# Optimization experiments

Hardware: AMD Instinct MI355X
Metric: run time of the kernel (lower is better)

## Reference

```python
import jax, jax.numpy as jnp
import numpy as np

R = 32
BN_EPS = 1e-5


def _bn(x, g, b):
    # eval-mode BatchNorm with running_mean=0, running_var=1
    shp = (1, -1) + (1,) * (x.ndim - 2)
    scale = g / np.float32(np.sqrt(1.0 + BN_EPS))
    return x * scale.reshape(shp) + b.reshape(shp)


def _conv3d(x, w, b):
    y = jax.lax.conv_general_dilated(x, w, (1, 1, 1), [(1, 1)] * 3,
                                     dimension_numbers=('NCDHW', 'OIDHW', 'NCDHW'))
    return y + b[None, :, None, None, None]


def _conv1d(x, w, b):  # kernel_size=1 conv -> matmul; w [O,I], x [B,I,N]
    return jnp.einsum('oi,bin->bon', w, x) + b[None, :, None]


def _voxelize(features, coords, r):
    # PVCNN Voxelization: detach coords, center, normalize, scatter-average
    coords = jax.lax.stop_gradient(coords)
    c = coords - coords.mean(axis=2, keepdims=True)            # [B,3,N]
    nrm = jnp.linalg.norm(c, axis=1, keepdims=True)            # [B,1,N]
    c = c / (nrm.max(axis=2, keepdims=True) * 2.0) + 0.5
    c = jnp.clip(c * r, 0.0, r - 1.0)                          # float voxel coords
    vox = jnp.round(c).astype(jnp.int32)
    B, C, N = features.shape
    idx = vox[:, 0] * r * r + vox[:, 1] * r + vox[:, 2]        # [B,N]
    flat = (idx + (jnp.arange(B, dtype=jnp.int32) * (r ** 3))[:, None]).reshape(-1)
    feats = features.transpose(0, 2, 1).reshape(B * N, C)
    sums = jax.ops.segment_sum(feats, flat, num_segments=B * r ** 3)
    cnt = jax.ops.segment_sum(jnp.ones((B * N,), features.dtype), flat, num_segments=B * r ** 3)
    grid = sums / jnp.maximum(cnt, 1.0)[:, None]
    grid = grid.reshape(B, r, r, r, C).transpose(0, 4, 1, 2, 3)  # [B,C,r,r,r]
    return grid, c


def _devoxelize(grid, c, r):
    # trilinear interpolation gather at float coords c in [0, r-1]
    B, C = grid.shape[:2]
    lo = jnp.clip(jnp.floor(c).astype(jnp.int32), 0, r - 1)
    hi = jnp.minimum(lo + 1, r - 1)
    f = c - lo.astype(c.dtype)
    gridf = grid.reshape(B, C, r * r * r)
    gather = jax.vmap(lambda g, i: g[:, i])  # per-batch [C,R3],[N] -> [C,N]
    out = jnp.zeros((B, C, c.shape[2]), grid.dtype)
    for ix, wx in ((lo[:, 0], 1.0 - f[:, 0]), (hi[:, 0], f[:, 0])):
        for iy, wy in ((lo[:, 1], 1.0 - f[:, 1]), (hi[:, 1], f[:, 1])):
            for iz, wz in ((lo[:, 2], 1.0 - f[:, 2]), (hi[:, 2], f[:, 2])):
                idx = ix * r * r + iy * r + iz
                out = out + gather(gridf, idx) * (wx * wy * wz)[:, None, :]
    return out


def setup_inputs() -> dict:
    key = jax.random.key(0)
    ks = jax.random.split(key, 24)
    n = lambda k, s, sc=0.05: (jax.random.normal(k, s, dtype=jnp.float32) * sc)
    inp = {
        'features': jax.random.normal(ks[0], (4, 64, 65536), dtype=jnp.float32),
        'coords': jax.random.normal(ks[1], (4, 3, 65536), dtype=jnp.float32),
        'vconv_w': n(ks[2], (64, 64, 3, 3, 3)),
        'vconv_b': n(ks[3], (64,)),
        'vbn_g': 1.0 + n(ks[4], (64,)),
        'vbn_b': n(ks[5], (64,)),
        'res_w': n(ks[6], (2, 2, 64, 64, 3, 3, 3)),
        'res_b': n(ks[7], (2, 2, 64)),
        'res_bn_g': 1.0 + n(ks[8], (2, 2, 64)),
        'res_bn_b': n(ks[9], (2, 2, 64)),
        'pf_w': n(ks[10], (64, 64)),
        'pf_b': n(ks[11], (64,)),
        'pf_bn_g': 1.0 + n(ks[12], (64,)),
        'pf_bn_b': n(ks[13], (64,)),
        'attn_wa': n(ks[14], (16, 64)),
        'attn_ba': n(ks[15], (16,)),
        'attn_wb': n(ks[16], (16, 64)),
        'attn_bb': n(ks[17], (16,)),
        'attn_wc': n(ks[18], (1, 32)),
        'attn_bc': n(ks[19], (1,)),
    }
    return inp


def reference(features, coords, vconv_w, vconv_b, vbn_g, vbn_b,
              res_w, res_b, res_bn_g, res_bn_b,
              pf_w, pf_b, pf_bn_g, pf_bn_b,
              attn_wa, attn_ba, attn_wb, attn_bb, attn_wc, attn_bc):
    grid, nc = _voxelize(features, coords, R)
    # BasicConvolutionBlock
    x = jax.nn.relu(_bn(_conv3d(grid, vconv_w, vconv_b), vbn_g, vbn_b))
    # two ResidualBlocks (inc==outc, stride 1 -> identity downsample)
    for i in range(2):
        y = jax.nn.relu(_bn(_conv3d(x, res_w[i, 0], res_b[i, 0]), res_bn_g[i, 0], res_bn_b[i, 0]))
        y = _bn(_conv3d(y, res_w[i, 1], res_b[i, 1]), res_bn_g[i, 1], res_bn_b[i, 1])
        x = jax.nn.relu(y + x)
    vfeat = _devoxelize(x, nc, R)                               # [B,64,N]
    # SharedMLP: Conv1d(k=1) + BN1d + ReLU
    pfeat = jax.nn.relu(_bn(_conv1d(features, pf_w, pf_b), pf_bn_g, pf_bn_b))
    # Attn fusion (channel dim 64 -> atten_64 branch)
    xa = _conv1d(vfeat, attn_wa, attn_ba)
    xb = _conv1d(pfeat, attn_wb, attn_bb)
    q = _conv1d(jnp.concatenate([xa, xb], axis=1), attn_wc, attn_bc)
    attention = 1.0 + jax.nn.sigmoid(q)
    fused = vfeat * attention + pfeat
    return fused
```

## Files before the change

kernel.cpp:

```cpp
#include <hip/hip_runtime.h>
#include <math.h>

#define NPT 65536
#define NB 4
#define R3 32768

typedef __attribute__((ext_vector_type(8))) short short8;
typedef __attribute__((ext_vector_type(16))) float f32x16;

#define OFF_WB16 0
#define OFF_BEFF 276480
#define OFF_PWB  276800
#define OFF_PB   280896
#define OFF_WAE  280960
#define OFF_WBE  281024
#define OFF_Q0   281088
#define OFF_MEAN 281104
#define OFF_MAXN 281116
#define OFF_PART 281120
#define OFF_AUX  281248
#define OFF_CB3  281504
#define OFF_CUR  1067936
#define OFF_ORD  1199008
#define OFF_GA   1330080
#define OFF_G0   9718688
#define OFF_G1   13912992

__device__ __forceinline__ unsigned short f2b(float f) {
    union { float f; unsigned int u; } v; v.f = f;
    unsigned int r = v.u + 0x7fffu + ((v.u >> 16) & 1u);
    return (unsigned short)(r >> 16);
}
__device__ __forceinline__ float b2f(unsigned short u) {
    union { unsigned int u; float f; } v; v.u = ((unsigned int)u) << 16; return v.f;
}

__global__ void k_setup(const float* __restrict__ vconv_w, const float* __restrict__ vconv_b,
                        const float* __restrict__ vbn_g, const float* __restrict__ vbn_b,
                        const float* __restrict__ res_w, const float* __restrict__ res_b,
                        const float* __restrict__ res_bn_g, const float* __restrict__ res_bn_b,
                        const float* __restrict__ pf_w, const float* __restrict__ pf_b,
                        const float* __restrict__ pf_bn_g, const float* __restrict__ pf_bn_b,
                        const float* __restrict__ wa, const float* __restrict__ ba,
                        const float* __restrict__ wb, const float* __restrict__ bb,
                        const float* __restrict__ wc, const float* __restrict__ bc,
                        float* __restrict__ ws) {
    int idx = blockIdx.x * 256 + threadIdx.x;
    const float invs = rsqrtf(1.00001f);
    if (idx < 552960) {
        unsigned short* wb16 = (unsigned short*)(ws + OFF_WB16);
        int j = idx & 7;
        int l = (idx >> 3) & 63;
        int nh = (idx >> 9) & 1;
        int ks = (idx >> 10) & 3;
        int rest = idx >> 12;
        int t = rest % 27;
        int layer = rest / 27;
        int i = ks * 16 + ((l >> 5) << 3) + j;
        int o = nh * 32 + (l & 31);
        float scale, wsrc;
        if (layer == 0) {
            scale = vbn_g[o] * invs;
            wsrc = vconv_w[(o * 64 + i) * 27 + t];
        } else {
            scale = res_bn_g[(layer - 1) * 64 + o] * invs;
            wsrc = res_w[(size_t)(layer - 1) * 110592 + (o * 64 + i) * 27 + t];
        }
        wb16[idx] = f2b(wsrc * scale);
        return;
    }
    idx -= 552960;
    if (idx < 320) {
        int l = idx >> 6, o = idx & 63;
        float b_, g_, s_;
        if (l == 0) { b_ = vconv_b[o]; g_ = vbn_g[o]; s_ = vbn_b[o]; }
        else {
            b_ = res_b[(l - 1) * 64 + o];
            g_ = res_bn_g[(l - 1) * 64 + o];
            s_ = res_bn_b[(l - 1) * 64 + o];
        }
        ws[OFF_BEFF + idx] = b_ * g_ * invs + s_;
    } else if (idx < 4416) {
        int e = idx - 320;
        int j = e & 7;
        int lane = (e >> 3) & 63;
        int ks = (e >> 9) & 3;
        int half = e >> 11;
        int i = ks * 16 + ((lane >> 5) << 3) + j;
        int o = half * 32 + (lane & 31);
        ((unsigned short*)(ws + OFF_PWB))[e] = f2b(pf_w[o * 64 + i] * pf_bn_g[o] * invs);
    } else if (idx < 4480) {
        int o = idx - 4416;
        ws[OFF_PB + o] = pf_b[o] * pf_bn_g[o] * invs + pf_bn_b[o];
    } else if (idx < 4544) {
        int o = idx - 4480;
        float s = 0.f;
        for (int j = 0; j < 16; j++) s += wc[j] * wa[j * 64 + o];
        ws[OFF_WAE + o] = s;
    } else if (idx < 4608) {
        int o = idx - 4544;
        float s = 0.f;
        for (int j = 0; j < 16; j++) s += wc[16 + j] * wb[j * 64 + o];
        ws[OFF_WBE + o] = s;
    } else if (idx == 4608) {
        float s = bc[0];
        for (int j = 0; j < 16; j++) s += wc[j] * ba[j] + wc[16 + j] * bb[j];
        ws[OFF_Q0] = s;
    }
}

__global__ __launch_bounds__(256) void k_mean1(const float* __restrict__ coords,
                                               float* __restrict__ part,
                                               float4* __restrict__ curz) {
    for (int i = blockIdx.x * 256 + threadIdx.x; i < 32768; i += 96 * 256)
        curz[i] = make_float4(0.f, 0.f, 0.f, 0.f);
    __shared__ float sm[256];
    int bd = blockIdx.x >> 3, chunk = blockIdx.x & 7;
    int tid = threadIdx.x;
    const float* p = coords + (size_t)bd * NPT + chunk * 8192;
    float s = 0.f;
    for (int n = tid; n < 8192; n += 256) s += p[n];
    sm[tid] = s; __syncthreads();
    for (int st = 128; st > 0; st >>= 1) {
        if (tid < st) sm[tid] += sm[tid + st];
        __syncthreads();
    }
    if (tid == 0) part[blockIdx.x] = sm[0];
}

__global__ __launch_bounds__(256) void k_maxn1(const float* __restrict__ coords,
                                               float* __restrict__ part,
                                               float* __restrict__ mean) {
    __shared__ float sm[256];
    int b = blockIdx.x >> 3, chunk = blockIdx.x & 7;
    int tid = threadIdx.x;
    float m0 = 0.f, m1 = 0.f, m2 = 0.f;
    #pragma unroll
    for (int c = 0; c < 8; c++) {
        m0 += part[(b * 3 + 0) * 8 + c];
        m1 += part[(b * 3 + 1) * 8 + c];
        m2 += part[(b * 3 + 2) * 8 + c];
    }
    m0 *= (1.0f / NPT); m1 *= (1.0f / NPT); m2 *= (1.0f / NPT);
    if (chunk == 0 && tid == 0) {
        mean[b * 3] = m0; mean[b * 3 + 1] = m1; mean[b * 3 + 2] = m2;
    }
    const float* p0 = coords + (size_t)(b * 3) * NPT + chunk * 8192;
    float mx = 0.f;
    for (int n = tid; n < 8192; n += 256) {
        float dx = p0[n] - m0, dy = p0[NPT + n] - m1, dz = p0[2 * NPT + n] - m2;
        mx = fmaxf(mx, dx * dx + dy * dy + dz * dz);
    }
    sm[tid] = mx; __syncthreads();
    for (int st = 128; st > 0; st >>= 1) {
        if (tid < st) sm[tid] = fmaxf(sm[tid], sm[tid + st]);
        __syncthreads();
    }
    if (tid == 0) part[96 + blockIdx.x] = sm[0];
}

__global__ void k_prep(const float* __restrict__ coords, const float* __restrict__ mean,
                       const float* __restrict__ part, float* __restrict__ cb3,
                       int* __restrict__ cursor) {
    int gid = blockIdx.x * 256 + threadIdx.x;
    int b = gid >> 16, n = gid & 65535;
    float mx = 0.f;
    #pragma unroll
    for (int c = 0; c < 8; c++) mx = fmaxf(mx, part[96 + b * 8 + c]);
    float inv = 0.5f / sqrtf(mx);
    float c0 = (coords[(size_t)(b * 3) * NPT + n]     - mean[b * 3])     * inv + 0.5f;
    float c1 = (coords[(size_t)(b * 3 + 1) * NPT + n] - mean[b * 3 + 1]) * inv + 0.5f;
    float c2 = (coords[(size_t)(b * 3 + 2) * NPT + n] - mean[b * 3 + 2]) * inv + 0.5f;
    c0 = fminf(fmaxf(c0 * 32.f, 0.f), 31.f);
    c1 = fminf(fmaxf(c1 * 32.f, 0.f), 31.f);
    c2 = fminf(fmaxf(c2 * 32.f, 0.f), 31.f);
    cb3[gid * 3]     = c0;
    cb3[gid * 3 + 1] = c1;
    cb3[gid * 3 + 2] = c2;
    int vx = b * R3 + ((int)rintf(c0) * 1024 + (int)rintf(c1) * 32 + (int)rintf(c2));
    atomicAdd(&cursor[vx], 1);
}

__global__ void k_scan1(int* __restrict__ cur, int* __restrict__ aux) {
    __shared__ int sm[256];
    int t = threadIdx.x;
    int base = blockIdx.x * 512 + t * 2;
    int c0 = cur[base], c1 = cur[base + 1];
    int s = c0 + c1;
    sm[t] = s; __syncthreads();
    for (int off = 1; off < 256; off <<= 1) {
        int v = (t >= off) ? sm[t - off] : 0;
        __syncthreads();
        sm[t] += v;
        __syncthreads();
    }
    int ex = sm[t] - s;
    cur[base] = ex;
    cur[base + 1] = ex + c0;
    if (t == 255) aux[blockIdx.x] = sm[t];
}

__global__ void k_scan3(int* __restrict__ cur, const int* __restrict__ aux) {
    __shared__ int sm[256];
    int t = threadIdx.x;
    sm[t] = (t < blockIdx.x) ? aux[t] : 0;
    __syncthreads();
    for (int off = 128; off > 0; off >>= 1) {
        if (t < off) sm[t] += sm[t + off];
        __syncthreads();
    }
    int add = sm[0];
    int base = blockIdx.x * 512 + t * 2;
    cur[base] += add;
    cur[base + 1] += add;
}

__global__ __launch_bounds__(256) void k_trans(const float* __restrict__ feats,
                                               unsigned short* __restrict__ ft) {
    __shared__ float lds[64][65];
    int b = blockIdx.x >> 10;
    int n0 = (blockIdx.x & 1023) << 6;
    int tid = threadIdx.x;
    int nl = tid & 63;
    #pragma unroll
    for (int it = 0; it < 16; it++) {
        int ch = it * 4 + (tid >> 6);
        lds[nl][ch] = feats[((size_t)(b * 64 + ch) << 16) + n0 + nl];
    }
    __syncthreads();
    int nn = tid >> 2;
    int ch0 = (tid & 3) << 4;
    size_t obase = (((size_t)(b << 16) + n0 + nn) << 6) + ch0;
    short8 v0, v1;
    #pragma unroll
    for (int j = 0; j < 8; j++) v0[j] = (short)f2b(lds[nn][ch0 + j]);
    #pragma unroll
    for (int j = 0; j < 8; j++) v1[j] = (short)f2b(lds[nn][ch0 + 8 + j]);
    *(short8*)(ft + obase) = v0;
    *(short8*)(ft + obase + 8) = v1;
}

__global__ void k_place(const float* __restrict__ cb3, int* __restrict__ cursor,
                        unsigned short* __restrict__ order) {
    int gid = blockIdx.x * 256 + threadIdx.x;
    int b = gid >> 16;
    float c0 = cb3[gid * 3], c1 = cb3[gid * 3 + 1], c2 = cb3[gid * 3 + 2];
    int vx = b * R3 + ((int)rintf(c0) * 1024 + (int)rintf(c1) * 32 + (int)rintf(c2));
    int slot = atomicAdd(&cursor[vx], 1);
    order[slot] = (unsigned short)(gid & 65535);
}

__global__ __launch_bounds__(256) void k_gather(const int* __restrict__ cursor,
        const unsigned short* __restrict__ order, const unsigned short* __restrict__ ft,
        unsigned short* __restrict__ g0) {
    int tid = threadIdx.x;
    int lane = tid & 63;
    int vx = blockIdx.x * 4 + (tid >> 6);
    int e = cursor[vx];
    int s = (vx == 0) ? 0 : cursor[vx - 1];
    int cnt = e - s;
    int p = lane >> 3;
    int g = lane & 7;
    int bb = vx >> 15;
    float acc[8] = {0.f, 0.f, 0.f, 0.f, 0.f, 0.f, 0.f, 0.f};
    for (int base = s; base < e; base += 8) {
        int idx = base + p;
        if (idx < e) {
            int n = order[idx];
            const unsigned short* fp = ft + (((size_t)(bb << 16) + n) << 6) + (g << 3);
            short8 v = *(const short8*)fp;
            #pragma unroll
            for (int j = 0; j < 8; j++) acc[j] += b2f((unsigned short)v[j]);
        }
    }
    #pragma unroll
    for (int j = 0; j < 8; j++) {
        acc[j] += __shfl_xor(acc[j], 8, 64);
        acc[j] += __shfl_xor(acc[j], 16, 64);
        acc[j] += __shfl_xor(acc[j], 32, 64);
    }
    if (p == 0) {
        float inv = 1.0f / (float)max(cnt, 1);
        int col = vx >> 5, z = vx & 31;
        short8 o8;
        #pragma unroll
        for (int j = 0; j < 8; j++) o8[j] = (short)f2b(acc[j] * inv);
        *(short8*)(g0 + (size_t)col * 2048 + (g << 8) + z * 8) = o8;
    }
}

__global__ __launch_bounds__(256) void k_conv(const unsigned short* __restrict__ in,
        const unsigned short* __restrict__ w, const float* __restrict__ bias,
        const float* __restrict__ idF, float* __restrict__ outF,
        unsigned short* __restrict__ out, int zmaj) {
    __shared__ unsigned short sA[18 * 2048];
    int tid = threadIdx.x;
    int lane = tid & 63;
    int wid = tid >> 6;
    int cp = wid & 1;
    int nh = wid >> 1;
    int tile = blockIdx.x;
    int b = blockIdx.y;
    int x = tile >> 3;
    int y0 = (tile & 7) << 2;
    #pragma unroll 1
    for (int s = 0; s < 18; s++) {
        int gx = x + s / 6 - 1;
        int gy = y0 + s % 6 - 1;
        if ((unsigned)gx < 32u && (unsigned)gy < 32u) {
            const unsigned short* gsrc = in + (((size_t)b * 1024 + gx * 32 + gy) << 11)
                                            + ((size_t)tid << 3);
            __builtin_amdgcn_global_load_lds(
                (const __attribute__((address_space(1))) unsigned int*)gsrc,
                (__attribute__((address_space(3))) unsigned int*)(sA + s * 2048 + (wid << 9)),
                16, 0, 0);
        } else {
            ((float4*)(sA + s * 2048))[tid] = make_float4(0.f, 0.f, 0.f, 0.f);
        }
    }
    __syncthreads();
    f32x16 accA = {}, accB = {};
    const short8 zero8 = {0, 0, 0, 0, 0, 0, 0, 0};
    int half = lane >> 5;
    int z = lane & 31;
    #pragma unroll 1
    for (int c9 = 0; c9 < 9; c9++) {
        int dxi = c9 / 3, dyi = c9 % 3;
        int s0 = dxi * 6 + dyi + cp * 2;
        const unsigned short* acol0 = sA + s0 * 2048 + (half << 8);
        const unsigned short* wbase = w + (dxi * 9 + dyi * 3) * 4096 + nh * 512 + lane * 8;
        #pragma unroll
        for (int dzi = 0; dzi < 3; dzi++) {
            int zz = z + dzi - 1;
            bool zv = (unsigned)zz < 32u;
            int zc = zv ? zz : 0;
            const unsigned short* ac0 = acol0 + zc * 8;
            const unsigned short* wp = wbase + dzi * 4096;
            #pragma unroll
            for (int ks = 0; ks < 4; ks++) {
                short8 bf = *(const short8*)(wp + ks * 1024);
                short8 a0 = *(const short8*)(ac0 + ks * 512);
                short8 a1 = *(const short8*)(ac0 + 2048 + ks * 512);
                if (!zv) { a0 = zero8; a1 = zero8; }
                accA = __builtin_amdgcn_mfma_f32_32x32x16_bf16(a0, bf, accA, 0, 0, 0);
                accB = __builtin_amdgcn_mfma_f32_32x32x16_bf16(a1, bf, accB, 0, 0, 0);
            }
        }
    }
    int o = nh * 32 + (lane & 31);
    float bb = bias[o];
    #pragma unroll
    for (int cc = 0; cc < 2; cc++) {
        int outcol = b * 1024 + x * 32 + (y0 + cp * 2 + cc);
        size_t cbase = (size_t)outcol << 11;
        size_t obase = cbase + (size_t)((o >> 3) << 8) + (o & 7);
        const f32x16& acc = cc ? accB : accA;
        #pragma unroll
        for (int r = 0; r < 16; r++) {
            int zr = (r & 3) + ((r >> 2) << 3) + ((lane >> 5) << 2);
            size_t oe = obase + (size_t)zr * 8;
            float v = acc[r] + bb;
            if (idF) v += idF[oe];
            v = fmaxf(v, 0.f);
            if (zmaj) out[cbase + (size_t)zr * 64 + o] = f2b(v);
            else out[oe] = f2b(v);
            if (outF) outF[oe] = v;
        }
    }
}

__global__ __launch_bounds__(256) void k_pfeat(const float* __restrict__ feats,
        const float* __restrict__ pb, const unsigned short* __restrict__ pwb,
        unsigned short* __restrict__ pf) {
    int tid = threadIdx.x;
    int lane = tid & 63;
    int wv = tid >> 6;
    int tile = blockIdx.x * 4 + wv;
    int b = tile >> 11;
    int n0 = (tile & 2047) << 5;
    int m = lane & 31, kg = lane >> 5;
    const float* fb = feats + ((size_t)b << 22) + n0 + m;
    f32x16 acc0 = {}, acc1 = {};
    #pragma unroll
    for (int ks = 0; ks < 4; ks++) {
        short8 af;
        #pragma unroll
        for (int j = 0; j < 8; j++)
            af[j] = (short)f2b(fb[(size_t)(ks * 16 + kg * 8 + j) << 16]);
        short8 b0 = *(const short8*)(pwb + ((size_t)(ks * 64 + lane) << 3));
        short8 b1 = *(const short8*)(pwb + ((size_t)((4 + ks) * 64 + lane) << 3));
        acc0 = __builtin_amdgcn_mfma_f32_32x32x16_bf16(af, b0, acc0, 0, 0, 0);
        acc1 = __builtin_amdgcn_mfma_f32_32x32x16_bf16(af, b1, acc1, 0, 0, 0);
    }
    int och = lane & 31;
    float bias0 = pb[och], bias1 = pb[32 + och];
    #pragma unroll
    for (int r = 0; r < 16; r++) {
        int p = (r & 3) + ((r >> 2) << 3) + ((lane >> 5) << 2);
        size_t base = ((size_t)(b << 16) + n0 + p) << 6;
        pf[base + och]      = f2b(fmaxf(acc0[r] + bias0, 0.f));
        pf[base + 32 + och] = f2b(fmaxf(acc1[r] + bias1, 0.f));
    }
}

__global__ __launch_bounds__(256) void k_final(const float* __restrict__ cb3,
        const unsigned short* __restrict__ gb, const unsigned short* __restrict__ pfeat,
        const float* __restrict__ ws, float* __restrict__ out) {
    int tid = threadIdx.x;
    int lane = tid & 63;
    int g = lane >> 3;
    int p = lane & 7;
    int b = blockIdx.y;
    int n = (blockIdx.x << 5) + ((tid >> 6) << 3) + p;
    int gid = (b << 16) + n;
    float c0 = cb3[gid * 3], c1 = cb3[gid * 3 + 1], c2 = cb3[gid * 3 + 2];
    int lx = (int)floorf(c0), ly = (int)floorf(c1), lz = (int)floorf(c2);
    int hx = min(lx + 1, 31), hy = min(ly + 1, 31), hz = min(lz + 1, 31);
    float fx = c0 - (float)lx, fy = c1 - (float)ly, fz = c2 - (float)lz;
    int xs[2] = {lx, hx}; float wxx[2] = {1.f - fx, fx};
    int ys[2] = {ly, hy}; float wyy[2] = {1.f - fy, fy};
    int zs[2] = {lz, hz}; float wzz[2] = {1.f - fz, fz};
    float vf[8];
    #pragma unroll
    for (int j = 0; j < 8; j++) vf[j] = 0.f;
    #pragma unroll
    for (int ii = 0; ii < 2; ii++)
    #pragma unroll
    for (int jj = 0; jj < 2; jj++)
    #pragma unroll
    for (int kk = 0; kk < 2; kk++) {
        float wgt = wxx[ii] * wyy[jj] * wzz[kk];
        const unsigned short* gp = gb + (((size_t)b * 1024 + xs[ii] * 32 + ys[jj]) << 11)
                                      + zs[kk] * 64 + (g << 3);
        short8 v = *(const short8*)gp;
        #pragma unroll
        for (int j = 0; j < 8; j++) vf[j] += wgt * b2f((unsigned short)v[j]);
    }
    float pfv[8];
    const unsigned short* pp = pfeat + ((size_t)gid << 6) + (g << 3);
    short8 pv = *(const short8*)pp;
    #pragma unroll
    for (int j = 0; j < 8; j++) pfv[j] = b2f((unsigned short)pv[j]);
    const float* wae = ws + OFF_WAE + (g << 3);
    const float* wbe = ws + OFF_WBE + (g << 3);
    float part = 0.f;
    #pragma unroll
    for (int j = 0; j < 8; j++) part += wae[j] * vf[j] + wbe[j] * pfv[j];
    part += __shfl_xor(part, 8, 64);
    part += __shfl_xor(part, 16, 64);
    part += __shfl_xor(part, 32, 64);
    float q = part + ws[OFF_Q0];
    float attn = 1.0f + 1.0f / (1.0f + expf(-q));
    float* op = out + (((size_t)(b * 64 + (g << 3))) << 16) + n;
    #pragma unroll
    for (int j = 0; j < 8; j++) op[(size_t)j << 16] = vf[j] * attn + pfv[j];
}

extern "C" void kernel_launch(void* const* d_in, const int* in_sizes, int n_in,
                              void* d_out, int out_size, void* d_ws, size_t ws_size,
                              hipStream_t stream) {
    const float* features = (const float*)d_in[0];
    const float* coords   = (const float*)d_in[1];
    const float* vconv_w  = (const float*)d_in[2];
    const float* vconv_b  = (const float*)d_in[3];
    const float* vbn_g    = (const float*)d_in[4];
    const float* vbn_b    = (const float*)d_in[5];
    const float* res_w    = (const float*)d_in[6];
    const float* res_b    = (const float*)d_in[7];
    const float* res_bn_g = (const float*)d_in[8];
    const float* res_bn_b = (const float*)d_in[9];
    const float* pf_w     = (const float*)d_in[10];
    const float* pf_b     = (const float*)d_in[11];
    const float* pf_bn_g  = (const float*)d_in[12];
    const float* pf_bn_b  = (const float*)d_in[13];
    const float* attn_wa  = (const float*)d_in[14];
    const float* attn_ba  = (const float*)d_in[15];
    const float* attn_wb  = (const float*)d_in[16];
    const float* attn_bb  = (const float*)d_in[17];
    const float* attn_wc  = (const float*)d_in[18];
    const float* attn_bc  = (const float*)d_in[19];
    float* ws  = (float*)d_ws;
    float* out = (float*)d_out;

    unsigned short* WB  = (unsigned short*)(ws + OFF_WB16);
    unsigned short* PWB = (unsigned short*)(ws + OFF_PWB);
    int*            CUR = (int*)(ws + OFF_CUR);
    int*            AUX = (int*)(ws + OFF_AUX);
    unsigned short* ORD = (unsigned short*)(ws + OFF_ORD);
    unsigned short* FT  = (unsigned short*)(ws + OFF_GA);
    unsigned short* PF  = (unsigned short*)(ws + OFF_GA);
    float* GA = ws + OFF_GA;
    unsigned short* G0 = (unsigned short*)(ws + OFF_G0);
    unsigned short* G1 = (unsigned short*)(ws + OFF_G1);
    const float* Bv = ws + OFF_BEFF;

    k_setup<<<2179, 256, 0, stream>>>(vconv_w, vconv_b, vbn_g, vbn_b, res_w, res_b,
                                      res_bn_g, res_bn_b, pf_w, pf_b, pf_bn_g, pf_bn_b,
                                      attn_wa, attn_ba, attn_wb, attn_bb, attn_wc, attn_bc, ws);
    k_mean1<<<96, 256, 0, stream>>>(coords, ws + OFF_PART, (float4*)CUR);
    k_maxn1<<<32, 256, 0, stream>>>(coords, ws + OFF_PART, ws + OFF_MEAN);
    k_prep<<<1024, 256, 0, stream>>>(coords, ws + OFF_MEAN, ws + OFF_PART,
                                     ws + OFF_CB3, CUR);
    k_scan1<<<256, 256, 0, stream>>>(CUR, AUX);
    k_scan3<<<256, 256, 0, stream>>>(CUR, AUX);
    k_trans<<<4096, 256, 0, stream>>>(features, FT);
    k_place<<<1024, 256, 0, stream>>>(ws + OFF_CB3, CUR, ORD);
    k_gather<<<32768, 256, 0, stream>>>(CUR, ORD, FT, G0);

    dim3 cg(256, 4);
    k_conv<<<cg, 256, 0, stream>>>(G0, WB + 0 * 110592, Bv + 0,   nullptr, GA,      G1, 0);
    k_conv<<<cg, 256, 0, stream>>>(G1, WB + 1 * 110592, Bv + 64,  nullptr, nullptr, G0, 0);
    k_conv<<<cg, 256, 0, stream>>>(G0, WB + 2 * 110592, Bv + 128, GA,      GA,      G1, 0);
    k_conv<<<cg, 256, 0, stream>>>(G1, WB + 3 * 110592, Bv + 192, nullptr, nullptr, G0, 0);
    k_conv<<<cg, 256, 0, stream>>>(G0, WB + 4 * 110592, Bv + 256, GA,      nullptr, G1, 1);

    k_pfeat<<<2048, 256, 0, stream>>>(features, ws + OFF_PB, PWB, PF);

    dim3 fg(2048, 4);
    k_final<<<fg, 256, 0, stream>>>(ws + OFF_CB3, G1, PF, ws, out);
}
```

Before: 535.4 us.

## Split conv K across wave pairs with 2x2 MFMA register tile and LDS reduction

Waves now split the input-channel dimension in half instead of the output-channel dimension. Each wave computes a 2x2 block of MFMA accumulators (two columns by two output halves), so every A and B fragment load feeds two MFMAs. The partial sums are then exchanged and reduced through LDS. Weights are re-laid out so both output halves load as adjacent short8 pairs, and invalid z taps read a zeroed LDS pad rather than using a select. This aims to cut LDS and global weight traffic per MFMA, at the cost of more accumulator registers and an extra reduction step with two barriers.

Measured after the change: 568.9 us. 1.06x slower.

```diff
diff --git a/kernel.cpp b/kernel.cpp
--- a/kernel.cpp
+++ b/kernel.cpp
@@ -50,8 +50,8 @@
     if (idx < 552960) {
         unsigned short* wb16 = (unsigned short*)(ws + OFF_WB16);
         int j = idx & 7;
-        int l = (idx >> 3) & 63;
-        int nh = (idx >> 9) & 1;
+        int nh = (idx >> 3) & 1;
+        int l = (idx >> 4) & 63;
         int ks = (idx >> 10) & 3;
         int rest = idx >> 12;
         int t = rest % 27;
@@ -293,16 +293,17 @@
         const unsigned short* __restrict__ w, const float* __restrict__ bias,
         const float* __restrict__ idF, float* __restrict__ outF,
         unsigned short* __restrict__ out, int zmaj) {
-    __shared__ unsigned short sA[18 * 2048];
+    __shared__ unsigned short sA[37384];
     int tid = threadIdx.x;
     int lane = tid & 63;
     int wid = tid >> 6;
     int cp = wid & 1;
-    int nh = wid >> 1;
+    int kh = wid >> 1;
     int tile = blockIdx.x;
     int b = blockIdx.y;
     int x = tile >> 3;
     int y0 = (tile & 7) << 2;
+    if (tid < 8) ((float*)sA)[18432 + (tid & 3) + ((tid >> 2) << 8)] = 0.f;
     #pragma unroll 1
     for (int s = 0; s < 18; s++) {
         int gx = x + s / 6 - 1;
@@ -319,42 +320,71 @@
         }
     }
     __syncthreads();
-    f32x16 accA = {}, accB = {};
-    const short8 zero8 = {0, 0, 0, 0, 0, 0, 0, 0};
+    f32x16 acc00 = {}, acc01 = {}, acc10 = {}, acc11 = {};
     int half = lane >> 5;
     int z = lane & 31;
+    int loff = half * 256 + z * 8 + kh * 1024;
+    const unsigned short* wl = w + lane * 16 + kh * 2048;
     #pragma unroll 1
     for (int c9 = 0; c9 < 9; c9++) {
         int dxi = c9 / 3, dyi = c9 % 3;
-        int s0 = dxi * 6 + dyi + cp * 2;
-        const unsigned short* acol0 = sA + s0 * 2048 + (half << 8);
-        const unsigned short* wbase = w + (dxi * 9 + dyi * 3) * 4096 + nh * 512 + lane * 8;
+        int sbase = (dxi * 6 + dyi + cp * 2) * 2048;
+        const unsigned short* wp0 = wl + c9 * 12288;
         #pragma unroll
         for (int dzi = 0; dzi < 3; dzi++) {
             int zz = z + dzi - 1;
             bool zv = (unsigned)zz < 32u;
-            int zc = zv ? zz : 0;
-            const unsigned short* ac0 = acol0 + zc * 8;
-            const unsigned short* wp = wbase + dzi * 4096;
+            int offd = loff + (dzi - 1) * 8;
+            int a0off = zv ? (sbase + offd) : 36864;
+            int a1off = zv ? (sbase + 2048 + offd) : 36864;
+            const unsigned short* wp = wp0 + dzi * 4096;
             #pragma unroll
-            for (int ks = 0; ks < 4; ks++) {
-                short8 bf = *(const short8*)(wp + ks * 1024);
-                short8 a0 = *(const short8*)(ac0 + ks * 512);
-                short8 a1 = *(const short8*)(ac0 + 2048 + ks * 512);
-                if (!zv) { a0 = zero8; a1 = zero8; }
-                accA = __builtin_amdgcn_mfma_f32_32x32x16_bf16(a0, bf, accA, 0, 0, 0);
-                accB = __builtin_amdgcn_mfma_f32_32x32x16_bf16(a1, bf, accB, 0, 0, 0);
+            for (int q = 0; q < 2; q++) {
+                short8 b0 = *(const short8*)(wp + q * 1024);
+                short8 b1 = *(const short8*)(wp + q * 1024 + 8);
+                short8 a0 = *(const short8*)(sA + a0off + q * 512);
+                short8 a1 = *(const short8*)(sA + a1off + q * 512);
+                acc00 = __builtin_amdgcn_mfma_f32_32x32x16_bf16(a0, b0, acc00, 0, 0, 0);
+                acc01 = __builtin_amdgcn_mfma_f32_32x32x16_bf16(a0, b1, acc01, 0, 0, 0);
+                acc10 = __builtin_amdgcn_mfma_f32_32x32x16_bf16(a1, b0, acc10, 0, 0, 0);
+                acc11 = __builtin_amdgcn_mfma_f32_32x32x16_bf16(a1, b1, acc11, 0, 0, 0);
             }
         }
     }
-    int o = nh * 32 + (lane & 31);
+    __syncthreads();
+    float* RED = (float*)sA;
+    {
+        const f32x16& p0 = kh ? acc00 : acc01;
+        const f32x16& p1 = kh ? acc10 : acc11;
+        int nhw = 1 - kh;
+        #pragma unroll
+        for (int rb = 0; rb < 4; rb++) {
+            float4 v0 = make_float4(p0[rb * 4], p0[rb * 4 + 1], p0[rb * 4 + 2], p0[rb * 4 + 3]);
+            float4 v1 = make_float4(p1[rb * 4], p1[rb * 4 + 1], p1[rb * 4 + 2], p1[rb * 4 + 3]);
+            ((float4*)(RED + ((((cp * 2 + nhw) * 2 + 0) * 4 + rb) << 8)))[lane] = v0;
+            ((float4*)(RED + ((((cp * 2 + nhw) * 2 + 1) * 4 + rb) << 8)))[lane] = v1;
+        }
+    }
+    __syncthreads();
+    f32x16 f0 = kh ? acc01 : acc00;
+    f32x16 f1 = kh ? acc11 : acc10;
+    #pragma unroll
+    for (int rb = 0; rb < 4; rb++) {
+        float4 v0 = ((float4*)(RED + ((((cp * 2 + kh) * 2 + 0) * 4 + rb) << 8)))[lane];
+        float4 v1 = ((float4*)(RED + ((((cp * 2 + kh) * 2 + 1) * 4 + rb) << 8)))[lane];
+        f0[rb * 4]     += v0.x; f0[rb * 4 + 1] += v0.y;
+        f0[rb * 4 + 2] += v0.z; f0[rb * 4 + 3] += v0.w;
+        f1[rb * 4]     += v1.x; f1[rb * 4 + 1] += v1.y;
+        f1[rb * 4 + 2] += v1.z; f1[rb * 4 + 3] += v1.w;
+    }
+    int o = kh * 32 + (lane & 31);
     float bb = bias[o];
     #pragma unroll
     for (int cc = 0; cc < 2; cc++) {
         int outcol = b * 1024 + x * 32 + (y0 + cp * 2 + cc);
         size_t cbase = (size_t)outcol << 11;
         size_t obase = cbase + (size_t)((o >> 3) << 8) + (o & 7);
-        const f32x16& acc = cc ? accB : accA;
+        const f32x16& acc = cc ? f1 : f0;
         #pragma unroll
         for (int r = 0; r < 16; r++) {
             int zr = (r & 3) + ((r >> 2) << 3) + ((lane >> 5) << 2);
```

## Split conv K dimension across two wave groups with LDS reduction

Applied to the files above, without the earlier changes.

The 3D conv kernel now launches 512 threads per block. Two groups of four waves each handle half of the input-channel reduction (ks 0-1 vs 2-3), and the halo staging loads are split between them. The second group writes its partial MFMA accumulators to shared memory, and the first group adds them before the bias, residual and ReLU epilogue. This doubles the waves available to hide latency in each tile, at the cost of an extra barrier and an LDS round-trip for the partial sums.

Measured after the change: 528.9 us. Within noise of the previous version (-1.2%).

```diff
diff --git a/kernel.cpp b/kernel.cpp
--- a/kernel.cpp
+++ b/kernel.cpp
@@ -289,7 +289,7 @@
     }
 }
 
-__global__ __launch_bounds__(256) void k_conv(const unsigned short* __restrict__ in,
+__global__ __launch_bounds__(512, 4) void k_conv(const unsigned short* __restrict__ in,
         const unsigned short* __restrict__ w, const float* __restrict__ bias,
         const float* __restrict__ idF, float* __restrict__ outF,
         unsigned short* __restrict__ out, int zmaj) {
@@ -298,24 +298,29 @@
     int lane = tid & 63;
     int wid = tid >> 6;
     int cp = wid & 1;
-    int nh = wid >> 1;
+    int nh = (wid >> 1) & 1;
+    int kh = wid >> 2;
     int tile = blockIdx.x;
     int b = blockIdx.y;
     int x = tile >> 3;
     int y0 = (tile & 7) << 2;
+    int t = tid & 255;
+    int h = tid >> 8;
+    int sq = wid & 3;
     #pragma unroll 1
-    for (int s = 0; s < 18; s++) {
+    for (int s2 = 0; s2 < 9; s2++) {
+        int s = s2 * 2 + h;
         int gx = x + s / 6 - 1;
         int gy = y0 + s % 6 - 1;
         if ((unsigned)gx < 32u && (unsigned)gy < 32u) {
             const unsigned short* gsrc = in + (((size_t)b * 1024 + gx * 32 + gy) << 11)
-                                            + ((size_t)tid << 3);
+                                            + ((size_t)t << 3);
             __builtin_amdgcn_global_load_lds(
                 (const __attribute__((address_space(1))) unsigned int*)gsrc,
-                (__attribute__((address_space(3))) unsigned int*)(sA + s * 2048 + (wid << 9)),
+                (__attribute__((address_space(3))) unsigned int*)(sA + s * 2048 + (sq << 9)),
                 16, 0, 0);
         } else {
-            ((float4*)(sA + s * 2048))[tid] = make_float4(0.f, 0.f, 0.f, 0.f);
+            ((float4*)(sA + s * 2048))[t] = make_float4(0.f, 0.f, 0.f, 0.f);
         }
     }
     __syncthreads();
@@ -327,8 +332,9 @@
     for (int c9 = 0; c9 < 9; c9++) {
         int dxi = c9 / 3, dyi = c9 % 3;
         int s0 = dxi * 6 + dyi + cp * 2;
-        const unsigned short* acol0 = sA + s0 * 2048 + (half << 8);
-        const unsigned short* wbase = w + (dxi * 9 + dyi * 3) * 4096 + nh * 512 + lane * 8;
+        const unsigned short* acol0 = sA + s0 * 2048 + (half << 8) + kh * 1024;
+        const unsigned short* wbase = w + (dxi * 9 + dyi * 3) * 4096 + nh * 512
+                                        + kh * 2048 + lane * 8;
         #pragma unroll
         for (int dzi = 0; dzi < 3; dzi++) {
             int zz = z + dzi - 1;
@@ -337,34 +343,59 @@
             const unsigned short* ac0 = acol0 + zc * 8;
             const unsigned short* wp = wbase + dzi * 4096;
             #pragma unroll
-            for (int ks = 0; ks < 4; ks++) {
-                short8 bf = *(const short8*)(wp + ks * 1024);
-                short8 a0 = *(const short8*)(ac0 + ks * 512);
-                short8 a1 = *(const short8*)(ac0 + 2048 + ks * 512);
+            for (int ksi = 0; ksi < 2; ksi++) {
+                short8 bf = *(const short8*)(wp + ksi * 1024);
+                short8 a0 = *(const short8*)(ac0 + ksi * 512);
+                short8 a1 = *(const short8*)(ac0 + 2048 + ksi * 512);
                 if (!zv) { a0 = zero8; a1 = zero8; }
                 accA = __builtin_amdgcn_mfma_f32_32x32x16_bf16(a0, bf, accA, 0, 0, 0);
                 accB = __builtin_amdgcn_mfma_f32_32x32x16_bf16(a1, bf, accB, 0, 0, 0);
             }
         }
     }
-    int o = nh * 32 + (lane & 31);
-    float bb = bias[o];
-    #pragma unroll
-    for (int cc = 0; cc < 2; cc++) {
-        int outcol = b * 1024 + x * 32 + (y0 + cp * 2 + cc);
-        size_t cbase = (size_t)outcol << 11;
-        size_t obase = cbase + (size_t)((o >> 3) << 8) + (o & 7);
-        const f32x16& acc = cc ? accB : accA;
-        #pragma unroll
-        for (int r = 0; r < 16; r++) {
-            int zr = (r & 3) + ((r >> 2) << 3) + ((lane >> 5) << 2);
-            size_t oe = obase + (size_t)zr * 8;
-            float v = acc[r] + bb;
-            if (idF) v += idF[oe];
-            v = fmaxf(v, 0.f);
-            if (zmaj) out[cbase + (size_t)zr * 64 + o] = f2b(v);
-            else out[oe] = f2b(v);
-            if (outF) outF[oe] = v;
+    __syncthreads();
+    float* RED = (float*)sA;
+    if (kh == 1) {
+        #pragma unroll
+        for (int c = 0; c < 2; c++) {
+            const f32x16& a = c ? accB : accA;
+            #pragma unroll
+            for (int rb = 0; rb < 4; rb++) {
+                float4 v = make_float4(a[rb * 4], a[rb * 4 + 1], a[rb * 4 + 2], a[rb * 4 + 3]);
+                ((float4*)(RED + ((((cp * 2 + nh) * 2 + c) * 4 + rb) << 8)))[lane] = v;
+            }
+        }
+    }
+    __syncthreads();
+    if (kh == 0) {
+        #pragma unroll
+        for (int rb = 0; rb < 4; rb++) {
+            float4 v0 = ((float4*)(RED + ((((cp * 2 + nh) * 2 + 0) * 4 + rb) << 8)))[lane];
+            float4 v1 = ((float4*)(RED + ((((cp * 2 + nh) * 2 + 1) * 4 + rb) << 8)))[lane];
+            accA[rb * 4]     += v0.x; accA[rb * 4 + 1] += v0.y;
+            accA[rb * 4 + 2] += v0.z; accA[rb * 4 + 3] += v0.w;
+            accB[rb * 4]     += v1.x; accB[rb * 4 + 1] += v1.y;
+            accB[rb * 4 + 2] += v1.z; accB[rb * 4 + 3] += v1.w;
+        }
+        int o = nh * 32 + (lane & 31);
+        float bb = bias[o];
+        #pragma unroll
+        for (int cc = 0; cc < 2; cc++) {
+            int outcol = b * 1024 + x * 32 + (y0 + cp * 2 + cc);
+            size_t cbase = (size_t)outcol << 11;
+            size_t obase = cbase + (size_t)((o >> 3) << 8) + (o & 7);
+            const f32x16& acc = cc ? accB : accA;
+            #pragma unroll
+            for (int r = 0; r < 16; r++) {
+                int zr = (r & 3) + ((r >> 2) << 3) + ((lane >> 5) << 2);
+                size_t oe = obase + (size_t)zr * 8;
+                float v = acc[r] + bb;
+                if (idF) v += idF[oe];
+                v = fmaxf(v, 0.f);
+                if (zmaj) out[cbase + (size_t)zr * 64 + o] = f2b(v);
+                else out[oe] = f2b(v);
+                if (outF) outF[oe] = v;
+            }
         }
     }
 }
@@ -508,11 +539,11 @@
     k_gather<<<32768, 256, 0, stream>>>(CUR, ORD, FT, G0);
 
     dim3 cg(256, 4);
-    k_conv<<<cg, 256, 0, stream>>>(G0, WB + 0 * 110592, Bv + 0,   nullptr, GA,      G1, 0);
-    k_conv<<<cg, 256, 0, stream>>>(G1, WB + 1 * 110592, Bv + 64,  nullptr, nullptr, G0, 0);
-    k_conv<<<cg, 256, 0, stream>>>(G0, WB + 2 * 110592, Bv + 128, GA,      GA,      G1, 0);
-    k_conv<<<cg, 256, 0, stream>>>(G1, WB + 3 * 110592, Bv + 192, nullptr, nullptr, G0, 0);
-    k_conv<<<cg, 256, 0, stream>>>(G0, WB + 4 * 110592, Bv + 256, GA,      nullptr, G1, 1);
+    k_conv<<<cg, 512, 0, stream>>>(G0, WB + 0 * 110592, Bv + 0,   nullptr, GA,      G1, 0);
+    k_conv<<<cg, 512, 0, stream>>>(G1, WB + 1 * 110592, Bv + 64,  nullptr, nullptr, G0, 0);
+    k_conv<<<cg, 512, 0, stream>>>(G0, WB + 2 * 110592, Bv + 128, GA,      GA,      G1, 0);
+    k_conv<<<cg, 512, 0, stream>>>(G1, WB + 3 * 110592, Bv + 192, nullptr, nullptr, G0, 0);
+    k_conv<<<cg, 512, 0, stream>>>(G0, WB + 4 * 110592, Bv + 256, GA,      nullptr, G1, 1);
 
     k_pfeat<<<2048, 256, 0, stream>>>(features, ws + OFF_PB, PWB, PF);
 
```
